# Kernel optimization log

Hardware: AMD Instinct MI355X
Metric: run time of the kernel (lower is better)

## Reference

```python
import jax, jax.numpy as jnp
import numpy as np

DIM = 768
HEADS = 12
HEAD_DIM = DIM // HEADS
SCALE = HEAD_DIM ** -0.5


def setup_inputs() -> dict:
    key = jax.random.key(0)
    ks = jax.random.split(key, 6)
    B, N, M, C = 4, 2048, 1024, DIM
    x = jax.random.normal(ks[0], (B, N, C), dtype=jnp.float32)
    r = jax.random.normal(ks[1], (B, M, C), dtype=jnp.float32)
    s = 1.0 / np.sqrt(C)
    W_q = jax.random.normal(ks[2], (C, C), dtype=jnp.float32) * s
    W_kv = jax.random.normal(ks[3], (C, 2 * C), dtype=jnp.float32) * s
    W_proj = jax.random.normal(ks[4], (C, C), dtype=jnp.float32) * s
    b_proj = jax.random.normal(ks[5], (C,), dtype=jnp.float32) * 0.02
    return {"x": x, "r": r, "W_q": W_q, "W_kv": W_kv, "W_proj": W_proj, "b_proj": b_proj}


def reference(x, r, W_q, W_kv, W_proj, b_proj):
    B, N, C = x.shape
    _, M, _ = r.shape
    H, D = HEADS, C // HEADS
    # projections (no bias on q/kv per qkv_bias=False)
    q = (x @ W_q).reshape(B, N, H, D)            # bnhd
    kv = (r @ W_kv).reshape(B, M, 2, H, D)
    k = kv[:, :, 0]                               # bmhd
    v = kv[:, :, 1]                               # bmhd
    attn = jnp.einsum('bnhd,bmhd->bhnm', q, k) * SCALE
    attn = jax.nn.softmax(attn, axis=-1)
    out = jnp.einsum('bhnm,bmhd->bnhd', attn, v).reshape(B, N, C)
    return out @ W_proj + b_proj
```

## Files before the change

kernel.cpp:

```cpp
#include <hip/hip_runtime.h>
#include <hip/hip_bf16.h>
#include <cstdint>

#define HEADS 12

typedef __attribute__((ext_vector_type(8))) __bf16 bf16x8;
typedef __attribute__((ext_vector_type(4))) __bf16 bf16x4;
typedef __attribute__((ext_vector_type(4))) float f32x4;

#define AS1 __attribute__((address_space(1)))
#define AS3 __attribute__((address_space(3)))

__device__ __forceinline__ void gload16(const void* src, void* lds) {
  __builtin_amdgcn_global_load_lds((AS1 void*)src, (AS3 void*)lds, 16, 0, 0);
}

__device__ __forceinline__ uint32_t cvtpk(float lo, float hi) {
  uint32_t r;
  asm("v_cvt_pk_bf16_f32 %0, %1, %2" : "=v"(r) : "v"(lo), "v"(hi));
  return r;
}

__device__ __forceinline__ float exp2_fast(float x) {
  float r;
  asm("v_exp_f32 %0, %1" : "=v"(r) : "v"(x));
  return r;
}

__global__ void k_cast2(const float* __restrict__ x, const float* __restrict__ r,
                        __bf16* __restrict__ xb, __bf16* __restrict__ rb) {
  int i = (blockIdx.x * 256 + threadIdx.x) * 4;
  const float* src;
  __bf16* dst;
  int off;
  if (i < 6291456) { src = x; dst = xb; off = i; }
  else             { src = r; dst = rb; off = i - 6291456; }
  float4 v = *(const float4*)(src + off);
  bf16x4 o;
  o[0] = (__bf16)v.x; o[1] = (__bf16)v.y; o[2] = (__bf16)v.z; o[3] = (__bf16)v.w;
  *(bf16x4*)(dst + off) = o;
}

__global__ void k_twc3(const float* __restrict__ Wq, const float* __restrict__ Wkv,
                       const float* __restrict__ Wp, __bf16* __restrict__ wqt,
                       __bf16* __restrict__ wkvt, __bf16* __restrict__ wpt) {
  __shared__ float tile[32][33];
  const float* W; __bf16* Wt; int N; float scale;
  if (blockIdx.z == 0)      { W = Wq;  Wt = wqt;  N = 768;  scale = 0.18033688011112042f; }
  else if (blockIdx.z == 1) { W = Wkv; Wt = wkvt; N = 1536; scale = 1.0f; }
  else                      { W = Wp;  Wt = wpt;  N = 768;  scale = 1.0f; }
  int nt = blockIdx.x, kt = blockIdx.y;
  if (nt * 32 >= N) return;
  int c = threadIdx.x & 31, r0 = threadIdx.x >> 5;
#pragma unroll
  for (int i = 0; i < 4; ++i) {
    int r = r0 + i * 8;
    tile[r][c] = W[(size_t)(kt * 32 + r) * N + nt * 32 + c];
  }
  __syncthreads();
#pragma unroll
  for (int i = 0; i < 4; ++i) {
    int r = r0 + i * 8;
    Wt[(size_t)(nt * 32 + r) * 768 + kt * 32 + c] = (__bf16)(tile[c][r] * scale);
  }
}

template<bool BF16OUT>
__global__ __launch_bounds__(256, 2) void k_gemm(
    const __bf16* __restrict__ A, const __bf16* __restrict__ Bt,
    void* __restrict__ C, const float* __restrict__ bias, __bf16* __restrict__ vTp,
    int M, int N, int K) {
  __shared__ __align__(16) char ldsA[2][16384];
  __shared__ __align__(16) char ldsB[2][16384];
  const int tid = threadIdx.x;
  const int ln = tid & 63;
  const int w = tid >> 6;
  const int nwx = gridDim.x;
  int bid = blockIdx.y * nwx + blockIdx.x;
  const int cpx = (nwx * gridDim.y) >> 3;
  bid = (bid & 7) * cpx + (bid >> 3);
  const int bm0 = (bid / nwx) * 128, bn0 = (bid % nwx) * 128;
  const int wm0 = (w >> 1) * 64, wn0 = (w & 1) * 64;

  auto stage = [&](char* lds, const __bf16* G, int row0, int k0) {
    const char* gb = (const char*)(G + (size_t)row0 * K + k0);
#pragma unroll
    for (int c = 0; c < 4; ++c) {
      int off = c * 4096 + tid * 16;
      int row = off >> 7;
      int s = ((off >> 4) & 7) ^ (row & 7);
      gload16(gb + (size_t)row * (K * 2) + (s << 4), lds + c * 4096 + (w << 10));
    }
  };

  f32x4 acc[4][4] = {};
  const int NK = K >> 6;
  stage(ldsA[0], A, bm0, 0);
  stage(ldsB[0], Bt, bn0, 0);
  __syncthreads();
  for (int kt = 0; kt < NK; ++kt) {
    const char* bufA = ldsA[kt & 1];
    const char* bufB = ldsB[kt & 1];
    if (kt + 1 < NK) {
      stage(ldsA[(kt + 1) & 1], A, bm0, (kt + 1) << 6);
      stage(ldsB[(kt + 1) & 1], Bt, bn0, (kt + 1) << 6);
    }
    bf16x8 af[2][4], bf[2][4];
#pragma unroll
    for (int kk = 0; kk < 2; ++kk)
#pragma unroll
      for (int mt = 0; mt < 4; ++mt) {
        int row = wm0 + mt * 16 + (ln & 15);
        af[kk][mt] = *(const bf16x8*)(bufA + row * 128 + (((kk * 4 + (ln >> 4)) ^ (row & 7)) << 4));
      }
#pragma unroll
    for (int kk = 0; kk < 2; ++kk)
#pragma unroll
      for (int nt = 0; nt < 4; ++nt) {
        int row = wn0 + nt * 16 + (ln & 15);
        bf[kk][nt] = *(const bf16x8*)(bufB + row * 128 + (((kk * 4 + (ln >> 4)) ^ (row & 7)) << 4));
      }
    __builtin_amdgcn_s_setprio(1);
#pragma unroll
    for (int kk = 0; kk < 2; ++kk)
#pragma unroll
      for (int mt = 0; mt < 4; ++mt)
#pragma unroll
        for (int nt = 0; nt < 4; ++nt)
          acc[mt][nt] = __builtin_amdgcn_mfma_f32_16x16x32_bf16(af[kk][mt], bf[kk][nt], acc[mt][nt], 0, 0, 0);
    __builtin_amdgcn_s_setprio(0);
    __syncthreads();
  }
#pragma unroll
  for (int mt = 0; mt < 4; ++mt) {
    int row = bm0 + wm0 + mt * 16 + ((ln >> 4) << 2);
#pragma unroll
    for (int nt = 0; nt < 4; ++nt) {
      int col = bn0 + wn0 + nt * 16 + (ln & 15);
      if (BF16OUT) {
        if (vTp != nullptr && bn0 >= 768) {
          bf16x4 o;
#pragma unroll
          for (int jj = 0; jj < 4; ++jj) o[jj] = (__bf16)acc[mt][nt][jj];
          *(bf16x4*)(vTp + ((size_t)((row >> 10) * 768 + col - 768)) * 1024 + (row & 1023)) = o;
        } else {
          __bf16* Cb = (__bf16*)C;
#pragma unroll
          for (int jj = 0; jj < 4; ++jj)
            Cb[(size_t)(row + jj) * N + col] = (__bf16)acc[mt][nt][jj];
        }
      } else {
        float* Cf = (float*)C;
        float bv = bias[col];
#pragma unroll
        for (int jj = 0; jj < 4; ++jj)
          Cf[(size_t)(row + jj) * N + col] = acc[mt][nt][jj] + bv;
      }
    }
  }
}

__global__ __launch_bounds__(512, 6) void k_attn(
    const __bf16* __restrict__ q, const __bf16* __restrict__ kv,
    const __bf16* __restrict__ vT, __bf16* __restrict__ ao) {
  __shared__ __align__(16) char ldsK[3][8192];
  __shared__ __align__(16) char ldsV[3][8192];
  const int tid = threadIdx.x, ln = tid & 63, w = tid >> 6, g = ln >> 4;
  const int qt = blockIdx.x, bh = blockIdx.y;
  const int b = bh / HEADS, h = bh % HEADS;
  const int qrow = b * 2048 + qt * 128 + w * 16 + (ln & 15);

  const char* kgb = (const char*)(kv + ((size_t)b * 1024) * 1536 + h * 64);
  const char* vgb = (const char*)(vT + ((size_t)(b * 768 + h * 64)) * 1024);

  const int srow = tid >> 3;
  const int scol = (((tid & 7) ^ (srow & 7)) << 4);
  const int ldst = w * 1024;

  auto stageKV = [&](int t, int buf) {
    gload16(kgb + (size_t)(t * 64 + srow) * 3072 + scol, ldsK[buf] + ldst);
    gload16(vgb + (size_t)srow * 2048 + (size_t)t * 128 + scol, ldsV[buf] + ldst);
  };

  bf16x8 qf[2];
#pragma unroll
  for (int kk = 0; kk < 2; ++kk)
    qf[kk] = *(const bf16x8*)(q + (size_t)qrow * 768 + h * 64 + (kk * 4 + g) * 8);

  stageKV(0, 0);
  stageKV(1, 1);

  f32x4 acc[4] = {};
  float mrow = -1e30f, lrow = 0.f;

  asm volatile("s_waitcnt vmcnt(2)" ::: "memory");
  __builtin_amdgcn_s_barrier();

  for (int t = 0; t < 16; ++t) {
    if (t < 14) stageKV(t + 2, (t + 2) % 3);
    const char* bufK = ldsK[t % 3];
    const char* bufV = ldsV[t % 3];

    f32x4 sf[4] = {};
    __builtin_amdgcn_s_setprio(1);
#pragma unroll
    for (int kk = 0; kk < 2; ++kk)
#pragma unroll
      for (int nt = 0; nt < 4; ++nt) {
        int row = nt * 16 + (ln & 15);
        bf16x8 kf = *(const bf16x8*)(bufK + row * 128 + (((kk * 4 + g) ^ (row & 7)) << 4));
        sf[nt] = __builtin_amdgcn_mfma_f32_16x16x32_bf16(kf, qf[kk], sf[nt], 0, 0, 0);
      }
    __builtin_amdgcn_s_setprio(0);

    float lm = sf[0][0];
#pragma unroll
    for (int nt = 0; nt < 4; ++nt)
#pragma unroll
      for (int jj = 0; jj < 4; ++jj) lm = fmaxf(lm, sf[nt][jj]);
    if (!__all(lm <= mrow + 8.0f)) {
      float mx = lm;
      mx = fmaxf(mx, __shfl_xor(mx, 16, 64));
      mx = fmaxf(mx, __shfl_xor(mx, 32, 64));
      float mn = fmaxf(mrow, mx);
      float corr = exp2_fast(mrow - mn);
      mrow = mn;
      lrow *= corr;
#pragma unroll
      for (int dt = 0; dt < 4; ++dt) acc[dt] *= corr;
    }
    float p[4][4];
    f32x4 ps = {0.f, 0.f, 0.f, 0.f};
#pragma unroll
    for (int nt = 0; nt < 4; ++nt)
#pragma unroll
      for (int jj = 0; jj < 4; ++jj) {
        float e = exp2_fast(sf[nt][jj] - mrow);
        p[nt][jj] = e;
        ps[jj] += e;
      }
    lrow += (ps[0] + ps[1]) + (ps[2] + ps[3]);

    bf16x8 pb[2];
    uint32_t c0[4], c1[4];
#pragma unroll
    for (int nt = 0; nt < 4; ++nt) {
      c0[nt] = cvtpk(p[nt][0], p[nt][1]);
      c1[nt] = cvtpk(p[nt][2], p[nt][3]);
    }
#pragma unroll
    for (int kk = 0; kk < 2; ++kk) {
      uint32_t x0 = c0[2 * kk], y0 = c0[2 * kk + 1];
      asm("v_permlane32_swap_b32 %0, %1" : "+v"(x0), "+v"(y0));
      asm("v_permlane16_swap_b32 %0, %1" : "+v"(x0), "+v"(y0));
      uint32_t x1 = c1[2 * kk], y1 = c1[2 * kk + 1];
      asm("v_permlane32_swap_b32 %0, %1" : "+v"(x1), "+v"(y1));
      asm("v_permlane16_swap_b32 %0, %1" : "+v"(x1), "+v"(y1));
      union { uint32_t u[4]; bf16x8 v; } pk;
      pk.u[0] = x0; pk.u[1] = x1; pk.u[2] = y0; pk.u[3] = y1;
      pb[kk] = pk.v;
    }

    __builtin_amdgcn_s_setprio(1);
#pragma unroll
    for (int kk = 0; kk < 2; ++kk)
#pragma unroll
      for (int dt = 0; dt < 4; ++dt) {
        int row = dt * 16 + (ln & 15);
        bf16x8 vf = *(const bf16x8*)(bufV + row * 128 + (((kk * 4 + g) ^ (row & 7)) << 4));
        acc[dt] = __builtin_amdgcn_mfma_f32_16x16x32_bf16(vf, pb[kk], acc[dt], 0, 0, 0);
      }
    __builtin_amdgcn_s_setprio(0);

    if (t < 14) {
      asm volatile("s_waitcnt vmcnt(2)" ::: "memory");
      __builtin_amdgcn_s_barrier();
    } else if (t == 14) {
      asm volatile("s_waitcnt vmcnt(0)" ::: "memory");
      __builtin_amdgcn_s_barrier();
    }
  }

  float l = lrow;
  l += __shfl_xor(l, 16, 64);
  l += __shfl_xor(l, 32, 64);
  float inv = 1.0f / l;
  size_t rowb = (size_t)qrow * 768 + h * 64;
#pragma unroll
  for (int dt = 0; dt < 4; ++dt) {
    bf16x4 o;
#pragma unroll
    for (int jj = 0; jj < 4; ++jj) o[jj] = (__bf16)(acc[dt][jj] * inv);
    *(bf16x4*)(ao + rowb + 16 * dt + 4 * g) = o;
  }
}

extern "C" void kernel_launch(void* const* d_in, const int* in_sizes, int n_in,
                              void* d_out, int out_size, void* d_ws, size_t ws_size,
                              hipStream_t stream) {
  const float* x = (const float*)d_in[0];
  const float* r = (const float*)d_in[1];
  const float* Wq = (const float*)d_in[2];
  const float* Wkv = (const float*)d_in[3];
  const float* Wp = (const float*)d_in[4];
  const float* bp = (const float*)d_in[5];

  char* ws = (char*)d_ws;
  __bf16* xb  = (__bf16*)ws; ws += (size_t)6291456 * 2;
  __bf16* rb  = (__bf16*)ws; ws += (size_t)3145728 * 2;
  __bf16* wqt = (__bf16*)ws; ws += (size_t)589824 * 2;
  __bf16* wkvt= (__bf16*)ws; ws += (size_t)1179648 * 2;
  __bf16* wpt = (__bf16*)ws; ws += (size_t)589824 * 2;
  __bf16* qb  = (__bf16*)ws; ws += (size_t)6291456 * 2;
  __bf16* kvb = (__bf16*)ws; ws += (size_t)6291456 * 2;
  __bf16* vT  = (__bf16*)ws; ws += (size_t)3145728 * 2;
  __bf16* ao  = (__bf16*)ws;

  k_cast2<<<9216, 256, 0, stream>>>(x, r, xb, rb);
  k_twc3<<<dim3(48, 24, 3), 256, 0, stream>>>(Wq, Wkv, Wp, wqt, wkvt, wpt);
  k_gemm<true><<<dim3(6, 64), 256, 0, stream>>>(xb, wqt, qb, nullptr, nullptr, 8192, 768, 768);
  k_gemm<true><<<dim3(12, 32), 256, 0, stream>>>(rb, wkvt, kvb, nullptr, vT, 4096, 1536, 768);
  k_attn<<<dim3(16, 48), 512, 0, stream>>>(qb, kvb, vT, ao);
  k_gemm<false><<<dim3(6, 64), 256, 0, stream>>>(ao, wpt, d_out, bp, nullptr, 8192, 768, 768);
}
```

Baseline: 112.2 us.

## Process two 16-row query tiles per wave in attention to reuse K/V fragments

Each wave in the attention kernel now handles 32 query rows, as two 16-row sub-tiles, instead of 16. Every K and V fragment read from LDS feeds two MFMAs, which halves LDS traffic and global K/V staging per query row. The grid is halved to 8x48 blocks and launch bounds drop to 4 waves-per-EU occupancy to leave room for the doubled accumulators and softmax state. The costs are higher register pressure, lower occupancy, and fewer blocks (384) to spread across the CUs.

```diff
diff --git a/kernel.cpp b/kernel.cpp
--- a/kernel.cpp
+++ b/kernel.cpp
@@ -160,7 +160,7 @@
   }
 }
 
-__global__ __launch_bounds__(512, 6) void k_attn(
+__global__ __launch_bounds__(512, 4) void k_attn(
     const __bf16* __restrict__ q, const __bf16* __restrict__ kv,
     const __bf16* __restrict__ vT, __bf16* __restrict__ ao) {
   __shared__ __align__(16) char ldsK[3][8192];
@@ -168,7 +168,7 @@
   const int tid = threadIdx.x, ln = tid & 63, w = tid >> 6, g = ln >> 4;
   const int qt = blockIdx.x, bh = blockIdx.y;
   const int b = bh / HEADS, h = bh % HEADS;
-  const int qrow = b * 2048 + qt * 128 + w * 16 + (ln & 15);
+  const int qbase = b * 2048 + qt * 256 + w * 32;
 
   const char* kgb = (const char*)(kv + ((size_t)b * 1024) * 1536 + h * 64);
   const char* vgb = (const char*)(vT + ((size_t)(b * 768 + h * 64)) * 1024);
@@ -182,16 +182,19 @@
     gload16(vgb + (size_t)srow * 2048 + (size_t)t * 128 + scol, ldsV[buf] + ldst);
   };
 
-  bf16x8 qf[2];
-#pragma unroll
-  for (int kk = 0; kk < 2; ++kk)
-    qf[kk] = *(const bf16x8*)(q + (size_t)qrow * 768 + h * 64 + (kk * 4 + g) * 8);
+  bf16x8 qf[2][2];
+#pragma unroll
+  for (int m = 0; m < 2; ++m)
+#pragma unroll
+    for (int kk = 0; kk < 2; ++kk)
+      qf[m][kk] = *(const bf16x8*)(q + (size_t)(qbase + m * 16 + (ln & 15)) * 768 + h * 64 + (kk * 4 + g) * 8);
 
   stageKV(0, 0);
   stageKV(1, 1);
 
-  f32x4 acc[4] = {};
-  float mrow = -1e30f, lrow = 0.f;
+  f32x4 acc[2][4] = {};
+  float mrow[2] = {-1e30f, -1e30f};
+  float lrow[2] = {0.f, 0.f};
 
   asm volatile("s_waitcnt vmcnt(2)" ::: "memory");
   __builtin_amdgcn_s_barrier();
@@ -201,7 +204,7 @@
     const char* bufK = ldsK[t % 3];
     const char* bufV = ldsV[t % 3];
 
-    f32x4 sf[4] = {};
+    f32x4 sf[2][4] = {};
     __builtin_amdgcn_s_setprio(1);
 #pragma unroll
     for (int kk = 0; kk < 2; ++kk)
@@ -209,56 +212,60 @@
       for (int nt = 0; nt < 4; ++nt) {
         int row = nt * 16 + (ln & 15);
         bf16x8 kf = *(const bf16x8*)(bufK + row * 128 + (((kk * 4 + g) ^ (row & 7)) << 4));
-        sf[nt] = __builtin_amdgcn_mfma_f32_16x16x32_bf16(kf, qf[kk], sf[nt], 0, 0, 0);
+        sf[0][nt] = __builtin_amdgcn_mfma_f32_16x16x32_bf16(kf, qf[0][kk], sf[0][nt], 0, 0, 0);
+        sf[1][nt] = __builtin_amdgcn_mfma_f32_16x16x32_bf16(kf, qf[1][kk], sf[1][nt], 0, 0, 0);
       }
     __builtin_amdgcn_s_setprio(0);
 
-    float lm = sf[0][0];
-#pragma unroll
-    for (int nt = 0; nt < 4; ++nt)
-#pragma unroll
-      for (int jj = 0; jj < 4; ++jj) lm = fmaxf(lm, sf[nt][jj]);
-    if (!__all(lm <= mrow + 8.0f)) {
-      float mx = lm;
-      mx = fmaxf(mx, __shfl_xor(mx, 16, 64));
-      mx = fmaxf(mx, __shfl_xor(mx, 32, 64));
-      float mn = fmaxf(mrow, mx);
-      float corr = exp2_fast(mrow - mn);
-      mrow = mn;
-      lrow *= corr;
-#pragma unroll
-      for (int dt = 0; dt < 4; ++dt) acc[dt] *= corr;
-    }
-    float p[4][4];
-    f32x4 ps = {0.f, 0.f, 0.f, 0.f};
-#pragma unroll
-    for (int nt = 0; nt < 4; ++nt)
-#pragma unroll
-      for (int jj = 0; jj < 4; ++jj) {
-        float e = exp2_fast(sf[nt][jj] - mrow);
-        p[nt][jj] = e;
-        ps[jj] += e;
-      }
-    lrow += (ps[0] + ps[1]) + (ps[2] + ps[3]);
-
-    bf16x8 pb[2];
-    uint32_t c0[4], c1[4];
-#pragma unroll
-    for (int nt = 0; nt < 4; ++nt) {
-      c0[nt] = cvtpk(p[nt][0], p[nt][1]);
-      c1[nt] = cvtpk(p[nt][2], p[nt][3]);
-    }
-#pragma unroll
-    for (int kk = 0; kk < 2; ++kk) {
-      uint32_t x0 = c0[2 * kk], y0 = c0[2 * kk + 1];
-      asm("v_permlane32_swap_b32 %0, %1" : "+v"(x0), "+v"(y0));
-      asm("v_permlane16_swap_b32 %0, %1" : "+v"(x0), "+v"(y0));
-      uint32_t x1 = c1[2 * kk], y1 = c1[2 * kk + 1];
-      asm("v_permlane32_swap_b32 %0, %1" : "+v"(x1), "+v"(y1));
-      asm("v_permlane16_swap_b32 %0, %1" : "+v"(x1), "+v"(y1));
-      union { uint32_t u[4]; bf16x8 v; } pk;
-      pk.u[0] = x0; pk.u[1] = x1; pk.u[2] = y0; pk.u[3] = y1;
-      pb[kk] = pk.v;
+    bf16x8 pb[2][2];
+#pragma unroll
+    for (int m = 0; m < 2; ++m) {
+      float lm = sf[m][0][0];
+#pragma unroll
+      for (int nt = 0; nt < 4; ++nt)
+#pragma unroll
+        for (int jj = 0; jj < 4; ++jj) lm = fmaxf(lm, sf[m][nt][jj]);
+      if (!__all(lm <= mrow[m] + 8.0f)) {
+        float mx = lm;
+        mx = fmaxf(mx, __shfl_xor(mx, 16, 64));
+        mx = fmaxf(mx, __shfl_xor(mx, 32, 64));
+        float mn = fmaxf(mrow[m], mx);
+        float corr = exp2_fast(mrow[m] - mn);
+        mrow[m] = mn;
+        lrow[m] *= corr;
+#pragma unroll
+        for (int dt = 0; dt < 4; ++dt) acc[m][dt] *= corr;
+      }
+      float p[4][4];
+      f32x4 ps = {0.f, 0.f, 0.f, 0.f};
+#pragma unroll
+      for (int nt = 0; nt < 4; ++nt)
+#pragma unroll
+        for (int jj = 0; jj < 4; ++jj) {
+          float e = exp2_fast(sf[m][nt][jj] - mrow[m]);
+          p[nt][jj] = e;
+          ps[jj] += e;
+        }
+      lrow[m] += (ps[0] + ps[1]) + (ps[2] + ps[3]);
+
+      uint32_t c0[4], c1[4];
+#pragma unroll
+      for (int nt = 0; nt < 4; ++nt) {
+        c0[nt] = cvtpk(p[nt][0], p[nt][1]);
+        c1[nt] = cvtpk(p[nt][2], p[nt][3]);
+      }
+#pragma unroll
+      for (int kk = 0; kk < 2; ++kk) {
+        uint32_t x0 = c0[2 * kk], y0 = c0[2 * kk + 1];
+        asm("v_permlane32_swap_b32 %0, %1" : "+v"(x0), "+v"(y0));
+        asm("v_permlane16_swap_b32 %0, %1" : "+v"(x0), "+v"(y0));
+        uint32_t x1 = c1[2 * kk], y1 = c1[2 * kk + 1];
+        asm("v_permlane32_swap_b32 %0, %1" : "+v"(x1), "+v"(y1));
+        asm("v_permlane16_swap_b32 %0, %1" : "+v"(x1), "+v"(y1));
+        union { uint32_t u[4]; bf16x8 v; } pk;
+        pk.u[0] = x0; pk.u[1] = x1; pk.u[2] = y0; pk.u[3] = y1;
+        pb[m][kk] = pk.v;
+      }
     }
 
     __builtin_amdgcn_s_setprio(1);
@@ -268,7 +275,8 @@
       for (int dt = 0; dt < 4; ++dt) {
         int row = dt * 16 + (ln & 15);
         bf16x8 vf = *(const bf16x8*)(bufV + row * 128 + (((kk * 4 + g) ^ (row & 7)) << 4));
-        acc[dt] = __builtin_amdgcn_mfma_f32_16x16x32_bf16(vf, pb[kk], acc[dt], 0, 0, 0);
+        acc[0][dt] = __builtin_amdgcn_mfma_f32_16x16x32_bf16(vf, pb[0][kk], acc[0][dt], 0, 0, 0);
+        acc[1][dt] = __builtin_amdgcn_mfma_f32_16x16x32_bf16(vf, pb[1][kk], acc[1][dt], 0, 0, 0);
       }
     __builtin_amdgcn_s_setprio(0);
 
@@ -281,17 +289,20 @@
     }
   }
 
-  float l = lrow;
-  l += __shfl_xor(l, 16, 64);
-  l += __shfl_xor(l, 32, 64);
-  float inv = 1.0f / l;
-  size_t rowb = (size_t)qrow * 768 + h * 64;
-#pragma unroll
-  for (int dt = 0; dt < 4; ++dt) {
-    bf16x4 o;
-#pragma unroll
-    for (int jj = 0; jj < 4; ++jj) o[jj] = (__bf16)(acc[dt][jj] * inv);
-    *(bf16x4*)(ao + rowb + 16 * dt + 4 * g) = o;
+#pragma unroll
+  for (int m = 0; m < 2; ++m) {
+    float l = lrow[m];
+    l += __shfl_xor(l, 16, 64);
+    l += __shfl_xor(l, 32, 64);
+    float inv = 1.0f / l;
+    size_t rowb = (size_t)(qbase + m * 16 + (ln & 15)) * 768 + h * 64;
+#pragma unroll
+    for (int dt = 0; dt < 4; ++dt) {
+      bf16x4 o;
+#pragma unroll
+      for (int jj = 0; jj < 4; ++jj) o[jj] = (__bf16)(acc[m][dt][jj] * inv);
+      *(bf16x4*)(ao + rowb + 16 * dt + 4 * g) = o;
+    }
   }
 }
 
@@ -320,6 +331,6 @@
   k_twc3<<<dim3(48, 24, 3), 256, 0, stream>>>(Wq, Wkv, Wp, wqt, wkvt, wpt);
   k_gemm<true><<<dim3(6, 64), 256, 0, stream>>>(xb, wqt, qb, nullptr, nullptr, 8192, 768, 768);
   k_gemm<true><<<dim3(12, 32), 256, 0, stream>>>(rb, wkvt, kvb, nullptr, vT, 4096, 1536, 768);
-  k_attn<<<dim3(16, 48), 512, 0, stream>>>(qb, kvb, vT, ao);
+  k_attn<<<dim3(8, 48), 512, 0, stream>>>(qb, kvb, vT, ao);
   k_gemm<false><<<dim3(6, 64), 256, 0, stream>>>(ao, wpt, d_out, bp, nullptr, 8192, 768, 768);
 }
```

After: 121.1 us. 8.0% more time.
